# Optimization experiments

Measured on AMD Instinct MI355X. Metric: run time of the kernel, lower is better.

## Reference

```python
import jax, jax.numpy as jnp
import numpy as np
from jax import lax

N, E = 10000, 100000
IN_CH, HID, EDGE_DIM, K = 32, 64, 16, 3
DILATIONS = (1, 2, 4)


def setup_inputs() -> dict:
    key = jax.random.key(0)
    ks = jax.random.split(key, 20)
    def nrm(k, shape, fan):
        return jax.random.normal(k, shape, jnp.float32) * (1.0 / np.sqrt(fan))
    inp = {
        "x": jax.random.normal(ks[0], (N, IN_CH), jnp.float32),
        "edge_attr": jax.random.normal(ks[1], (E, EDGE_DIM), jnp.float32),
        "h_prev": jax.random.normal(ks[2], (N, K, HID), jnp.float32),
        "edge_index": jax.random.randint(ks[3], (2, E), 0, N, jnp.int32),
        # edge-conditioning MLP: edge_dim -> 32 -> in_ch*hid
        "w1": nrm(ks[4], (EDGE_DIM, 32), EDGE_DIM), "b1": jnp.zeros((32,), jnp.float32),
        "w2": nrm(ks[5], (32, IN_CH * HID), 32), "b2": jnp.zeros((IN_CH * HID,), jnp.float32),
        # NNConv root weight + bias
        "root": nrm(ks[6], (IN_CH, HID), IN_CH), "bias": jnp.zeros((HID,), jnp.float32),
        # three dilated Conv1d layers [out, in, k]
        "tcn_w1": nrm(ks[7], (HID, HID, K), HID * K), "tcn_b1": jnp.zeros((HID,), jnp.float32),
        "tcn_w2": nrm(ks[8], (HID, HID, K), HID * K), "tcn_b2": jnp.zeros((HID,), jnp.float32),
        "tcn_w3": nrm(ks[9], (HID, HID, K), HID * K), "tcn_b3": jnp.zeros((HID,), jnp.float32),
        # output projection hid*3 -> hid
        "proj_w": nrm(ks[10], (HID * len(DILATIONS), HID), HID * len(DILATIONS)),
        "proj_b": jnp.zeros((HID,), jnp.float32),
    }
    return inp


def _conv1d_last(h, w, b, dilation):
    # h: [N, C, L], w: [O, I, K]; 'same'-style padding (K-1)*d//2, return last timestep.
    pad = (K - 1) * dilation // 2
    out = lax.conv_general_dilated(
        h, w, window_strides=(1,), padding=[(pad, pad)],
        rhs_dilation=(dilation,), dimension_numbers=("NCH", "OIH", "NCH"))
    return out[:, :, -1] + b[None, :]


def reference(x, edge_attr, h_prev, edge_index,
              w1, b1, w2, b2, root, bias,
              tcn_w1, tcn_b1, tcn_w2, tcn_b2, tcn_w3, tcn_b3,
              proj_w, proj_b):
    src, dst = edge_index[0], edge_index[1]
    n = x.shape[0]

    # --- NNConv (ECC): per-edge weight via MLP, gather -> matmul -> scatter-mean ---
    h_e = jax.nn.relu(edge_attr @ w1 + b1)                   # [E, 32]
    W_e = (h_e @ w2 + b2).reshape(-1, IN_CH, HID)            # [E, in, hid]
    msg = jnp.einsum("ei,eio->eo", x[src], W_e)             # [E, hid]
    agg = jax.ops.segment_sum(msg, dst, num_segments=n)      # [N, hid]
    cnt = jax.ops.segment_sum(jnp.ones((msg.shape[0],), msg.dtype), dst, num_segments=n)
    mean = agg / jnp.maximum(cnt, 1.0)[:, None]
    h_graph = jax.nn.relu(mean + x @ root + bias)            # [N, hid]

    # --- history update ---
    h_hist = jnp.concatenate([h_prev[:, 1:], h_graph[:, None, :]], axis=1)  # [N, K, hid]

    # --- dilated TCN stack, keep only last timestep of each branch ---
    h_in = jnp.transpose(h_hist, (0, 2, 1))                  # [N, hid, K]
    outs = [
        _conv1d_last(h_in, tcn_w1, tcn_b1, DILATIONS[0]),
        _conv1d_last(h_in, tcn_w2, tcn_b2, DILATIONS[1]),
        _conv1d_last(h_in, tcn_w3, tcn_b3, DILATIONS[2]),
    ]
    h_cat = jnp.concatenate(outs, axis=1)                    # [N, hid*3]
    h_out = h_cat @ proj_w + proj_b                          # dropout = identity (eval)
    return h_out, h_hist
```

## Files before the change

### kernel.cpp

```cpp
#include <hip/hip_runtime.h>
#include <stdint.h>

#define NN 10000
#define NE 100000
#define CHUNK 10

__device__ __forceinline__ float bu2f(uint16_t u) {
    return __uint_as_float(((uint32_t)u) << 16);
}
__device__ __forceinline__ float blo(uint32_t v) { return __uint_as_float(v << 16); }
__device__ __forceinline__ float bhi(uint32_t v) { return __uint_as_float(v & 0xffff0000u); }
__device__ __forceinline__ uint16_t f2bu(float f) {
    uint32_t u = __float_as_uint(f);
    return (uint16_t)((u + 0x7fffu + ((u >> 16) & 1u)) >> 16);
}
__device__ __forceinline__ float ldf(const void* p, size_t i, int f32) {
    return f32 ? ((const float*)p)[i] : bu2f(((const uint16_t*)p)[i]);
}
struct f8 { float v[8]; };
__device__ __forceinline__ f8 ldf8(const void* p, size_t i, int f32) {
    f8 r;
    if (f32) {
        const float4* q = (const float4*)((const float*)p + i);
        float4 a = q[0], b = q[1];
        r.v[0]=a.x; r.v[1]=a.y; r.v[2]=a.z; r.v[3]=a.w;
        r.v[4]=b.x; r.v[5]=b.y; r.v[6]=b.z; r.v[7]=b.w;
    } else {
        uint4 u = *(const uint4*)((const uint16_t*)p + i);
        r.v[0]=blo(u.x); r.v[1]=bhi(u.x); r.v[2]=blo(u.y); r.v[3]=bhi(u.y);
        r.v[4]=blo(u.z); r.v[5]=bhi(u.z); r.v[6]=blo(u.w); r.v[7]=bhi(u.w);
    }
    return r;
}
__device__ __forceinline__ void stf(void* p, size_t i, float v, int f32) {
    if (f32) ((float*)p)[i] = v;
    else ((uint16_t*)p)[i] = f2bu(v);
}
__device__ __forceinline__ int clampi(int v, int lo, int hi) {
    return min(max(v, lo), hi);
}

__global__ __launch_bounds__(256) void k_init(
    const void* __restrict__ x, float4* __restrict__ zbase, int* __restrict__ flag)
{
    __shared__ int red[256];
    int bid = blockIdx.x;
    int tid = threadIdx.x;
    if (bid < 657) {
        int idx = bid * 256 + tid;
        if (idx < 168088) zbase[idx] = make_float4(0.f, 0.f, 0.f, 0.f);
    } else {
        const uint16_t* p = (const uint16_t*)x;
        int c = 0;
        #pragma unroll
        for (int q = 0; q < 4; q++) {
            float a = fabsf(bu2f(p[tid + q * 256]));
            if (a > 1e-3f && a < 16.0f) c++;
        }
        red[tid] = c;
        __syncthreads();
        #pragma unroll
        for (int d = 128; d > 0; d >>= 1) {
            if (tid < d) red[tid] += red[tid + d];
            __syncthreads();
        }
        if (tid == 0) *flag = (red[0] < 870) ? 1 : 0;
    }
}

__global__ __launch_bounds__(256, 4) void k_prep(
    const void* __restrict__ x, const void* __restrict__ root,
    const void* __restrict__ tw1, const void* __restrict__ tw2,
    const void* __restrict__ tw3,
    const void* __restrict__ tb1, const void* __restrict__ tb2,
    const void* __restrict__ tb3,
    const void* __restrict__ proj_w,
    const void* __restrict__ edge_attr, const void* __restrict__ w1,
    const void* __restrict__ b1,
    const void* __restrict__ w2, const void* __restrict__ b2,
    const int* __restrict__ ei, const int* __restrict__ flag,
    float* __restrict__ xs_f, float* __restrict__ root_f,
    float* __restrict__ A, float* __restrict__ B, float* __restrict__ C,
    float* __restrict__ dv,
    int* __restrict__ outdeg, int* __restrict__ indeg, int* __restrict__ rank,
    uint16_t* __restrict__ h_edge,
    uint16_t* __restrict__ T, float* __restrict__ xb)
{
    int bid = blockIdx.x;
    int tid = threadIdx.x;
    __shared__ union PU {
        struct { float xs[8][32]; uint16_t Ts[32][64]; } t;
        struct { float w1s[512]; float b1s[32]; float eas[32][16]; } mlp;
    } su;

    if (bid < 1250) {
        int f32 = *flag;
        int n0 = bid * 8;
        if (tid < 32) {
            f8 r = ldf8(x, (size_t)n0 * 32 + (size_t)tid * 8, f32);
            int base = tid * 8;
            #pragma unroll
            for (int q = 0; q < 8; q++) su.t.xs[(base + q) >> 5][(base + q) & 31] = r.v[q];
        }
        __syncthreads();
        int j = tid >> 3;
        int o0 = (tid & 7) * 8;
        float acc[8][8];
        #pragma unroll
        for (int s = 0; s < 8; s++)
            #pragma unroll
            for (int r = 0; r < 8; r++) acc[s][r] = 0.0f;
        if (f32) {
            const float* wb = (const float*)w2 + (size_t)j * 2048 + o0;
            for (int i = 0; i < 32; i++) {
                float4 a4 = *(const float4*)(wb + i * 64);
                float4 b4 = *(const float4*)(wb + i * 64 + 4);
                #pragma unroll
                for (int s = 0; s < 8; s++) {
                    float xv = su.t.xs[s][i];
                    acc[s][0] = fmaf(xv, a4.x, acc[s][0]); acc[s][1] = fmaf(xv, a4.y, acc[s][1]);
                    acc[s][2] = fmaf(xv, a4.z, acc[s][2]); acc[s][3] = fmaf(xv, a4.w, acc[s][3]);
                    acc[s][4] = fmaf(xv, b4.x, acc[s][4]); acc[s][5] = fmaf(xv, b4.y, acc[s][5]);
                    acc[s][6] = fmaf(xv, b4.z, acc[s][6]); acc[s][7] = fmaf(xv, b4.w, acc[s][7]);
                }
            }
        } else {
            const uint16_t* wb = (const uint16_t*)w2 + (size_t)j * 2048 + o0;
            for (int i = 0; i < 32; i++) {
                uint4 u = *(const uint4*)(wb + i * 64);
                float w0 = blo(u.x), w1_ = bhi(u.x), w2_ = blo(u.y), w3 = bhi(u.y);
                float w4 = blo(u.z), w5 = bhi(u.z), w6 = blo(u.w), w7 = bhi(u.w);
                #pragma unroll
                for (int s = 0; s < 8; s++) {
                    float xv = su.t.xs[s][i];
                    acc[s][0] = fmaf(xv, w0, acc[s][0]); acc[s][1] = fmaf(xv, w1_, acc[s][1]);
                    acc[s][2] = fmaf(xv, w2_, acc[s][2]); acc[s][3] = fmaf(xv, w3, acc[s][3]);
                    acc[s][4] = fmaf(xv, w4, acc[s][4]); acc[s][5] = fmaf(xv, w5, acc[s][5]);
                    acc[s][6] = fmaf(xv, w6, acc[s][6]); acc[s][7] = fmaf(xv, w7, acc[s][7]);
                }
            }
        }
        int k = tid >> 6, o = tid & 63;
        #pragma unroll
        for (int s = 0; s < 8; s++) {
            uint4 ov;
            ov.x = ((uint32_t)f2bu(acc[s][1]) << 16) | f2bu(acc[s][0]);
            ov.y = ((uint32_t)f2bu(acc[s][3]) << 16) | f2bu(acc[s][2]);
            ov.z = ((uint32_t)f2bu(acc[s][5]) << 16) | f2bu(acc[s][4]);
            ov.w = ((uint32_t)f2bu(acc[s][7]) << 16) | f2bu(acc[s][6]);
            *(uint4*)&su.t.Ts[j][o0] = ov;
            __syncthreads();
            uint16_t v0 = su.t.Ts[k * 8 + 0][o];
            uint16_t v1 = su.t.Ts[k * 8 + 1][o];
            uint16_t v2 = su.t.Ts[k * 8 + 2][o];
            uint16_t v3 = su.t.Ts[k * 8 + 3][o];
            uint16_t v4 = su.t.Ts[k * 8 + 4][o];
            uint16_t v5 = su.t.Ts[k * 8 + 5][o];
            uint16_t v6 = su.t.Ts[k * 8 + 6][o];
            uint16_t v7 = su.t.Ts[k * 8 + 7][o];
            uint4 tv_;
            tv_.x = (uint32_t)v0 | ((uint32_t)v1 << 16);
            tv_.y = (uint32_t)v2 | ((uint32_t)v3 << 16);
            tv_.z = (uint32_t)v4 | ((uint32_t)v5 << 16);
            tv_.w = (uint32_t)v6 | ((uint32_t)v7 << 16);
            *(uint4*)(T + (size_t)(n0 + s) * 2048 + (size_t)o * 32 + k * 8) = tv_;
            __syncthreads();
        }
        {
            int oo = tid & 63;
            if (f32) {
                const float* b2f = (const float*)b2;
                #pragma unroll
                for (int h = 0; h < 2; h++) {
                    int s = (tid >> 6) + h * 4;
                    float a2 = 0.0f;
                    #pragma unroll
                    for (int i = 0; i < 32; i++)
                        a2 = fmaf(su.t.xs[s][i], b2f[i * 64 + oo], a2);
                    xb[(size_t)(n0 + s) * 64 + oo] = a2;
                }
            } else {
                const uint16_t* b2u = (const uint16_t*)b2;
                #pragma unroll
                for (int h = 0; h < 2; h++) {
                    int s = (tid >> 6) + h * 4;
                    float a2 = 0.0f;
                    #pragma unroll
                    for (int i = 0; i < 32; i++)
                        a2 = fmaf(su.t.xs[s][i], bu2f(b2u[i * 64 + oo]), a2);
                    xb[(size_t)(n0 + s) * 64 + oo] = a2;
                }
            }
        }
    } else if (bid < 4375) {
        int f32 = *flag;
        int e0 = (bid - 1250) * 32;
        if (tid < 64) {
            f8 r = ldf8(w1, (size_t)tid * 8, f32);
            #pragma unroll
            for (int q = 0; q < 8; q++) su.mlp.w1s[tid * 8 + q] = r.v[q];
        } else if (tid < 128) {
            int t = tid - 64;
            f8 r = ldf8(edge_attr, (size_t)e0 * 16 + (size_t)t * 8, f32);
            int el = t >> 1, half = (t & 1) * 8;
            #pragma unroll
            for (int q = 0; q < 8; q++) su.mlp.eas[el][half + q] = r.v[q];
        } else if (tid < 160) {
            su.mlp.b1s[tid - 128] = ldf(b1, tid - 128, f32);
        }
        __syncthreads();
        int el = tid >> 5, jj = tid & 31;
        float wreg[16];
        #pragma unroll
        for (int k = 0; k < 16; k++) wreg[k] = su.mlp.w1s[k * 32 + jj];
        float bj = su.mlp.b1s[jj];
        #pragma unroll
        for (int r = 0; r < 4; r++) {
            int e = el + r * 8;
            float acc = bj;
            #pragma unroll
            for (int k = 0; k < 16; k++) acc = fmaf(su.mlp.eas[e][k], wreg[k], acc);
            h_edge[(size_t)(e0 + e) * 32 + jj] = f2bu(fmaxf(acc, 0.0f));
        }
    } else if (bid < 4887) {
        int f32 = *flag;
        int beta = bid - 4375;
        int i = beta >> 3;
        int chunk = beta & 7;
        int o = tid & 63, sub = tid >> 6;
        int cc0 = chunk * 8 + sub * 2;
        float a = 0.f, b = 0.f, c = 0.f, d = 0.f;
        #pragma unroll
        for (int m = 0; m < 2; m++) {
            int cc = cc0 + m;
            float p0 = ldf(proj_w, (size_t)cc * 64 + o, f32);
            float p1 = ldf(proj_w, (size_t)(64 + cc) * 64 + o, f32);
            float p2 = ldf(proj_w, (size_t)(128 + cc) * 64 + o, f32);
            size_t base = (size_t)cc * 192 + i * 3;
            a = fmaf(ldf(tw1, base + 1, f32), p0, a);
            a = fmaf(ldf(tw2, base + 1, f32), p1, a);
            a = fmaf(ldf(tw3, base + 1, f32), p2, a);
            b = fmaf(ldf(tw2, base + 0, f32), p1, b);
            c = fmaf(ldf(tw1, base + 0, f32), p0, c);
            if (i == 0) {
                d = fmaf(ldf(tb1, cc, f32), p0, d);
                d = fmaf(ldf(tb2, cc, f32), p1, d);
                d = fmaf(ldf(tb3, cc, f32), p2, d);
            }
        }
        unsafeAtomicAdd(&A[i * 64 + o], a);
        unsafeAtomicAdd(&B[i * 64 + o], b);
        unsafeAtomicAdd(&C[i * 64 + o], c);
        if (i == 0) unsafeAtomicAdd(&dv[o], d);
    } else if (bid < 5278) {
        int e = (bid - 4887) * 256 + tid;
        if (e < NE) {
            int src = clampi(ei[e], 0, NN - 1);
            rank[e] = atomicAdd(&outdeg[src], 1);
            atomicAdd(&indeg[clampi(ei[NE + e], 0, NN - 1)], 1);
        }
    } else if (bid < 5435) {
        int f32 = *flag;
        int v8 = (bid - 5278) * 256 + tid;
        if (v8 < 40000) {
            f8 r = ldf8(x, (size_t)v8 * 8, f32);
            float4* o = (float4*)(xs_f + (size_t)v8 * 8);
            o[0] = make_float4(r.v[0], r.v[1], r.v[2], r.v[3]);
            o[1] = make_float4(r.v[4], r.v[5], r.v[6], r.v[7]);
        }
    } else {
        int f32 = *flag;
        f8 r = ldf8(root, (size_t)tid * 8, f32);
        float4* o = (float4*)(root_f + (size_t)tid * 8);
        o[0] = make_float4(r.v[0], r.v[1], r.v[2], r.v[3]);
        o[1] = make_float4(r.v[4], r.v[5], r.v[6], r.v[7]);
    }
}

__global__ __launch_bounds__(256) void k_scat(
    const int* __restrict__ ei, const int* __restrict__ outdeg,
    const int* __restrict__ rank,
    int* __restrict__ sorted_src, int* __restrict__ sorted_dst,
    int* __restrict__ sorted_eid,
    const uint16_t* __restrict__ h_edge, uint16_t* __restrict__ h_srt, int hs_mode)
{
    __shared__ int offs_l[NN];
    __shared__ int tsum[256];
    int tid = threadIdx.x;
    const int CH = 40;
    int base = tid * CH;
    int s = 0;
    for (int k = 0; k < CH; k++) {
        int i = base + k;
        if (i < NN) s += outdeg[i];
    }
    tsum[tid] = s;
    __syncthreads();
    for (int d = 1; d < 256; d <<= 1) {
        int t = (tid >= d) ? tsum[tid - d] : 0;
        __syncthreads();
        if (tid >= d) tsum[tid] += t;
        __syncthreads();
    }
    int run = (tid == 0) ? 0 : tsum[tid - 1];
    for (int k = 0; k < CH; k++) {
        int i = base + k;
        if (i < NN) { offs_l[i] = run; run += outdeg[i]; }
    }
    __syncthreads();
    #pragma unroll
    for (int r = 0; r < 4; r++) {
        int e = blockIdx.x * 1024 + r * 256 + tid;
        if (e < NE) {
            int src = clampi(ei[e], 0, NN - 1);
            int dst = clampi(ei[NE + e], 0, NN - 1);
            int pos = clampi(offs_l[src] + rank[e], 0, NE - 1);
            sorted_src[pos] = src;
            sorted_dst[pos] = dst;
            if (hs_mode) {
                const uint4* hs = (const uint4*)(h_edge + (size_t)e * 32);
                uint4* hd = (uint4*)(h_srt + (size_t)pos * 32);
                hd[0] = hs[0]; hd[1] = hs[1]; hd[2] = hs[2]; hd[3] = hs[3];
            } else {
                sorted_eid[pos] = e;
            }
        }
    }
}

__global__ __launch_bounds__(256) void k_msg_g(
    const uint16_t* __restrict__ h_edge, const uint16_t* __restrict__ h_srt,
    int hs_mode, const uint16_t* __restrict__ T,
    const float* __restrict__ xb, const int* __restrict__ sorted_src,
    const int* __restrict__ sorted_dst, const int* __restrict__ sorted_eid,
    float* __restrict__ agg)
{
    int wid = blockIdx.x * 4 + (threadIdx.x >> 6);
    int lane = threadIdx.x & 63;
    int p0 = wid * CHUNK;
    if (p0 >= NE) return;
    int p1 = min(p0 + CHUNK, NE);
    int cur = -1;
    float tv[32];
    float xbv = 0.0f;
    int sN = clampi(sorted_src[p0], 0, NN - 1);
    const uint4* hq;
    if (hs_mode) hq = (const uint4*)(h_srt + (size_t)p0 * 32);
    else hq = (const uint4*)(h_edge + (size_t)clampi(sorted_eid[p0], 0, NE - 1) * 32);
    uint4 na = hq[0], nb = hq[1], nc = hq[2], nd = hq[3];
    for (int p = p0; p < p1; p++) {
        int s = sN;
        uint4 a = na, b = nb, c = nc, d = nd;
        int dst = clampi(sorted_dst[p], 0, NN - 1);
        if (p + 1 < p1) {
            sN = clampi(sorted_src[p + 1], 0, NN - 1);
            const uint4* h2;
            if (hs_mode) h2 = (const uint4*)(h_srt + (size_t)(p + 1) * 32);
            else h2 = (const uint4*)(h_edge + (size_t)clampi(sorted_eid[p + 1], 0, NE - 1) * 32);
            na = h2[0]; nb = h2[1]; nc = h2[2]; nd = h2[3];
        }
        if (s != cur) {
            cur = s;
            const uint4* Tp = (const uint4*)(T + (size_t)s * 2048 + (size_t)lane * 32);
            uint4 t0 = Tp[0], t1 = Tp[1], t2 = Tp[2], t3 = Tp[3];
            tv[0]=blo(t0.x); tv[1]=bhi(t0.x); tv[2]=blo(t0.y); tv[3]=bhi(t0.y);
            tv[4]=blo(t0.z); tv[5]=bhi(t0.z); tv[6]=blo(t0.w); tv[7]=bhi(t0.w);
            tv[8]=blo(t1.x); tv[9]=bhi(t1.x); tv[10]=blo(t1.y); tv[11]=bhi(t1.y);
            tv[12]=blo(t1.z); tv[13]=bhi(t1.z); tv[14]=blo(t1.w); tv[15]=bhi(t1.w);
            tv[16]=blo(t2.x); tv[17]=bhi(t2.x); tv[18]=blo(t2.y); tv[19]=bhi(t2.y);
            tv[20]=blo(t2.z); tv[21]=bhi(t2.z); tv[22]=blo(t2.w); tv[23]=bhi(t2.w);
            tv[24]=blo(t3.x); tv[25]=bhi(t3.x); tv[26]=blo(t3.y); tv[27]=bhi(t3.y);
            tv[28]=blo(t3.z); tv[29]=bhi(t3.z); tv[30]=blo(t3.w); tv[31]=bhi(t3.w);
            xbv = xb[(size_t)s * 64 + lane];
        }
        float s0 = 0.f, s1 = 0.f, s2 = 0.f, s3 = 0.f;
        s0 = fmaf(blo(a.x), tv[0],  s0); s0 = fmaf(bhi(a.x), tv[1],  s0);
        s0 = fmaf(blo(a.y), tv[2],  s0); s0 = fmaf(bhi(a.y), tv[3],  s0);
        s0 = fmaf(blo(a.z), tv[4],  s0); s0 = fmaf(bhi(a.z), tv[5],  s0);
        s0 = fmaf(blo(a.w), tv[6],  s0); s0 = fmaf(bhi(a.w), tv[7],  s0);
        s1 = fmaf(blo(b.x), tv[8],  s1); s1 = fmaf(bhi(b.x), tv[9],  s1);
        s1 = fmaf(blo(b.y), tv[10], s1); s1 = fmaf(bhi(b.y), tv[11], s1);
        s1 = fmaf(blo(b.z), tv[12], s1); s1 = fmaf(bhi(b.z), tv[13], s1);
        s1 = fmaf(blo(b.w), tv[14], s1); s1 = fmaf(bhi(b.w), tv[15], s1);
        s2 = fmaf(blo(c.x), tv[16], s2); s2 = fmaf(bhi(c.x), tv[17], s2);
        s2 = fmaf(blo(c.y), tv[18], s2); s2 = fmaf(bhi(c.y), tv[19], s2);
        s2 = fmaf(blo(c.z), tv[20], s2); s2 = fmaf(bhi(c.z), tv[21], s2);
        s2 = fmaf(blo(c.w), tv[22], s2); s2 = fmaf(bhi(c.w), tv[23], s2);
        s3 = fmaf(blo(d.x), tv[24], s3); s3 = fmaf(bhi(d.x), tv[25], s3);
        s3 = fmaf(blo(d.y), tv[26], s3); s3 = fmaf(bhi(d.y), tv[27], s3);
        s3 = fmaf(blo(d.z), tv[28], s3); s3 = fmaf(bhi(d.z), tv[29], s3);
        s3 = fmaf(blo(d.w), tv[30], s3); s3 = fmaf(bhi(d.w), tv[31], s3);
        float acc = xbv + (s0 + s1) + (s2 + s3);
        unsafeAtomicAdd(&agg[(size_t)dst * 64 + lane], acc);
    }
}

__global__ __launch_bounds__(256) void k_node_out(
    const float* __restrict__ agg, const int* __restrict__ indeg,
    const float* __restrict__ xs_f, const float* __restrict__ root_f,
    const void* __restrict__ bias, const void* __restrict__ h_prev,
    const float* __restrict__ A, const float* __restrict__ B,
    const float* __restrict__ C, const float* __restrict__ dv,
    const void* __restrict__ proj_b,
    const int* __restrict__ flag, void* __restrict__ out)
{
    int f32 = *flag;
    int tid = threadIdx.x;
    int s = tid >> 6, o = tid & 63;
    int n = blockIdx.x * 4 + s;
    const size_t O1 = (size_t)NN * 64;
    __shared__ float hg_s[4][64], hp1_s[4][64], hp2_s[4][64];

    float xr = 0.0f;
    const float* xp = xs_f + (size_t)n * 32;
    #pragma unroll
    for (int i = 0; i < 32; i++)
        xr = fmaf(xp[i], root_f[i * 64 + o], xr);
    float c = (float)indeg[n];
    float m = agg[(size_t)n * 64 + o] / fmaxf(c, 1.0f);
    float hg = fmaxf(m + xr + ldf(bias, o, f32), 0.0f);
    float hp1 = ldf(h_prev, (size_t)n * 192 + 64 + o, f32);
    float hp2 = ldf(h_prev, (size_t)n * 192 + 128 + o, f32);
    hg_s[s][o] = hg; hp1_s[s][o] = hp1; hp2_s[s][o] = hp2;
    stf(out, O1 + (size_t)n * 192 + o, hp1, f32);
    stf(out, O1 + (size_t)n * 192 + 64 + o, hp2, f32);
    stf(out, O1 + (size_t)n * 192 + 128 + o, hg, f32);
    __syncthreads();

    float accA = 0.f, accB = 0.f, accC = 0.f;
    #pragma unroll 8
    for (int i = 0; i < 64; i++) {
        accA = fmaf(hg_s[s][i],  A[i * 64 + o], accA);
        accB = fmaf(hp1_s[s][i], B[i * 64 + o], accB);
        accC = fmaf(hp2_s[s][i], C[i * 64 + o], accC);
    }
    float acc = dv[o] + ldf(proj_b, o, f32) + (accA + accB) + accC;
    stf(out, (size_t)n * 64 + o, acc, f32);
}

static inline size_t align64(size_t v) { return (v + 63) & ~(size_t)63; }

extern "C" void kernel_launch(void* const* d_in, const int* in_sizes, int n_in,
                              void* d_out, int out_size, void* d_ws, size_t ws_size,
                              hipStream_t stream) {
    const void* x         = d_in[0];
    const void* edge_attr = d_in[1];
    const void* h_prev    = d_in[2];
    const int*  ei        = (const int*)d_in[3];
    const void* w1     = d_in[4];
    const void* b1     = d_in[5];
    const void* w2     = d_in[6];
    const void* b2     = d_in[7];
    const void* root   = d_in[8];
    const void* bias   = d_in[9];
    const void* tw1    = d_in[10];
    const void* tb1    = d_in[11];
    const void* tw2    = d_in[12];
    const void* tb2    = d_in[13];
    const void* tw3    = d_in[14];
    const void* tb3    = d_in[15];
    const void* proj_w = d_in[16];
    const void* proj_b = d_in[17];

    char* ws = (char*)d_ws;
    size_t off = 0;
    uint16_t* T      = (uint16_t*)(ws + off); off = align64(off + (size_t)NN * 2048 * 2);
    uint16_t* h_edge = (uint16_t*)(ws + off); off = align64(off + (size_t)NE * 32 * 2);
    float* xs_f   = (float*)(ws + off); off = align64(off + (size_t)NN * 32 * 4);
    float* root_f = (float*)(ws + off); off = align64(off + (size_t)2048 * 4);
    float* xb     = (float*)(ws + off); off = align64(off + (size_t)NN * 64 * 4);
    size_t zero_base = off;
    float* agg    = (float*)(ws + off); off = align64(off + (size_t)NN * 64 * 4);
    int* indeg    = (int*)(ws + off);   off = align64(off + (size_t)NN * 4);
    int* outdeg   = (int*)(ws + off);   off = align64(off + (size_t)NN * 4);
    float* Amat   = (float*)(ws + off); off = align64(off + (size_t)4096 * 4);
    float* Bmat   = (float*)(ws + off); off = align64(off + (size_t)4096 * 4);
    float* Cmat   = (float*)(ws + off); off = align64(off + (size_t)4096 * 4);
    float* dvec   = (float*)(ws + off); off = align64(off + (size_t)64 * 4);
    int* rank        = (int*)(ws + off); off = align64(off + (size_t)NE * 4);
    int* sorted_src  = (int*)(ws + off); off = align64(off + (size_t)NE * 4);
    int* sorted_dst  = (int*)(ws + off); off = align64(off + (size_t)NE * 4);
    int* sorted_eid  = (int*)(ws + off); off = align64(off + (size_t)NE * 4);
    int* flag        = (int*)(ws + off); off = align64(off + 64);
    uint16_t* h_srt  = (uint16_t*)(ws + off);
    size_t off_end = off + (size_t)NE * 32 * 2;
    int hs_mode = (off_end <= ws_size) ? 1 : 0;

    k_init<<<658, 256, 0, stream>>>(x, (float4*)((char*)d_ws + zero_base), flag);
    k_prep<<<5436, 256, 0, stream>>>(x, root, tw1, tw2, tw3, tb1, tb2, tb3,
                                     proj_w, edge_attr, w1, b1, w2, b2, ei, flag,
                                     xs_f, root_f, Amat, Bmat, Cmat, dvec,
                                     outdeg, indeg, rank, h_edge, T, xb);
    k_scat<<<(NE + 1023) / 1024, 256, 0, stream>>>(ei, outdeg, rank,
                                                   sorted_src, sorted_dst, sorted_eid,
                                                   h_edge, h_srt, hs_mode);
    k_msg_g<<<(NE / CHUNK + 3) / 4, 256, 0, stream>>>(h_edge, h_srt, hs_mode, T, xb,
                                                      sorted_src, sorted_dst,
                                                      sorted_eid, agg);
    k_node_out<<<NN / 4, 256, 0, stream>>>(agg, indeg, xs_f, root_f, bias, h_prev,
                                           Amat, Bmat, Cmat, dvec, proj_b, flag, d_out);
}
```

Before: 213.9 us.

## Drop sorted h_edge copy, prefetch T rows, double-buffer LDS transpose, widen MLP blocks

The scatter kernel no longer copies per-edge hidden vectors into sorted order. The message kernel now gathers h_edge through sorted_eid and prefetches the next source node's T row and xb value one edge ahead, so their load latency is hidden. The T-transpose stage double-buffers its shared-memory tile, which removes one barrier per iteration. The edge-MLP blocks now handle 64 edges each, with bounds checks, which cuts the prep grid size. The trade-off is that k_msg_g reads h_edge by random index instead of sequentially and holds more registers for the prefetched data.

```diff
diff --git a/kernel.cpp b/kernel.cpp
--- a/kernel.cpp
+++ b/kernel.cpp
@@ -89,8 +89,8 @@
     int bid = blockIdx.x;
     int tid = threadIdx.x;
     __shared__ union PU {
-        struct { float xs[8][32]; uint16_t Ts[32][64]; } t;
-        struct { float w1s[512]; float b1s[32]; float eas[32][16]; } mlp;
+        struct { float xs[8][32]; uint16_t Ts[2][32][64]; } t;
+        struct { float w1s[512]; float b1s[32]; float eas[64][16]; } mlp;
     } su;
 
     if (bid < 1250) {
@@ -148,23 +148,22 @@
             ov.y = ((uint32_t)f2bu(acc[s][3]) << 16) | f2bu(acc[s][2]);
             ov.z = ((uint32_t)f2bu(acc[s][5]) << 16) | f2bu(acc[s][4]);
             ov.w = ((uint32_t)f2bu(acc[s][7]) << 16) | f2bu(acc[s][6]);
-            *(uint4*)&su.t.Ts[j][o0] = ov;
+            *(uint4*)&su.t.Ts[s & 1][j][o0] = ov;
             __syncthreads();
-            uint16_t v0 = su.t.Ts[k * 8 + 0][o];
-            uint16_t v1 = su.t.Ts[k * 8 + 1][o];
-            uint16_t v2 = su.t.Ts[k * 8 + 2][o];
-            uint16_t v3 = su.t.Ts[k * 8 + 3][o];
-            uint16_t v4 = su.t.Ts[k * 8 + 4][o];
-            uint16_t v5 = su.t.Ts[k * 8 + 5][o];
-            uint16_t v6 = su.t.Ts[k * 8 + 6][o];
-            uint16_t v7 = su.t.Ts[k * 8 + 7][o];
+            uint16_t v0 = su.t.Ts[s & 1][k * 8 + 0][o];
+            uint16_t v1 = su.t.Ts[s & 1][k * 8 + 1][o];
+            uint16_t v2 = su.t.Ts[s & 1][k * 8 + 2][o];
+            uint16_t v3 = su.t.Ts[s & 1][k * 8 + 3][o];
+            uint16_t v4 = su.t.Ts[s & 1][k * 8 + 4][o];
+            uint16_t v5 = su.t.Ts[s & 1][k * 8 + 5][o];
+            uint16_t v6 = su.t.Ts[s & 1][k * 8 + 6][o];
+            uint16_t v7 = su.t.Ts[s & 1][k * 8 + 7][o];
             uint4 tv_;
             tv_.x = (uint32_t)v0 | ((uint32_t)v1 << 16);
             tv_.y = (uint32_t)v2 | ((uint32_t)v3 << 16);
             tv_.z = (uint32_t)v4 | ((uint32_t)v5 << 16);
             tv_.w = (uint32_t)v6 | ((uint32_t)v7 << 16);
             *(uint4*)(T + (size_t)(n0 + s) * 2048 + (size_t)o * 32 + k * 8) = tv_;
-            __syncthreads();
         }
         {
             int oo = tid & 63;
@@ -192,21 +191,27 @@
                 }
             }
         }
-    } else if (bid < 4375) {
+    } else if (bid < 2813) {
         int f32 = *flag;
-        int e0 = (bid - 1250) * 32;
+        int e0 = (bid - 1250) * 64;
         if (tid < 64) {
             f8 r = ldf8(w1, (size_t)tid * 8, f32);
             #pragma unroll
             for (int q = 0; q < 8; q++) su.mlp.w1s[tid * 8 + q] = r.v[q];
-        } else if (tid < 128) {
-            int t = tid - 64;
-            f8 r = ldf8(edge_attr, (size_t)e0 * 16 + (size_t)t * 8, f32);
-            int el = t >> 1, half = (t & 1) * 8;
-            #pragma unroll
-            for (int q = 0; q < 8; q++) su.mlp.eas[el][half + q] = r.v[q];
-        } else if (tid < 160) {
-            su.mlp.b1s[tid - 128] = ldf(b1, tid - 128, f32);
+        } else if (tid < 192) {
+            int tt = tid - 64;
+            size_t fo = (size_t)e0 * 16 + (size_t)tt * 8;
+            int el = tt >> 1, half = (tt & 1) * 8;
+            if (fo + 8 <= (size_t)NE * 16) {
+                f8 r = ldf8(edge_attr, fo, f32);
+                #pragma unroll
+                for (int q = 0; q < 8; q++) su.mlp.eas[el][half + q] = r.v[q];
+            } else {
+                #pragma unroll
+                for (int q = 0; q < 8; q++) su.mlp.eas[el][half + q] = 0.0f;
+            }
+        } else if (tid < 224) {
+            su.mlp.b1s[tid - 192] = ldf(b1, tid - 192, f32);
         }
         __syncthreads();
         int el = tid >> 5, jj = tid & 31;
@@ -215,16 +220,17 @@
         for (int k = 0; k < 16; k++) wreg[k] = su.mlp.w1s[k * 32 + jj];
         float bj = su.mlp.b1s[jj];
         #pragma unroll
-        for (int r = 0; r < 4; r++) {
+        for (int r = 0; r < 8; r++) {
             int e = el + r * 8;
             float acc = bj;
             #pragma unroll
             for (int k = 0; k < 16; k++) acc = fmaf(su.mlp.eas[e][k], wreg[k], acc);
-            h_edge[(size_t)(e0 + e) * 32 + jj] = f2bu(fmaxf(acc, 0.0f));
-        }
-    } else if (bid < 4887) {
+            if (e0 + e < NE)
+                h_edge[(size_t)(e0 + e) * 32 + jj] = f2bu(fmaxf(acc, 0.0f));
+        }
+    } else if (bid < 3325) {
         int f32 = *flag;
-        int beta = bid - 4375;
+        int beta = bid - 2813;
         int i = beta >> 3;
         int chunk = beta & 7;
         int o = tid & 63, sub = tid >> 6;
@@ -252,16 +258,16 @@
         unsafeAtomicAdd(&B[i * 64 + o], b);
         unsafeAtomicAdd(&C[i * 64 + o], c);
         if (i == 0) unsafeAtomicAdd(&dv[o], d);
-    } else if (bid < 5278) {
-        int e = (bid - 4887) * 256 + tid;
+    } else if (bid < 3716) {
+        int e = (bid - 3325) * 256 + tid;
         if (e < NE) {
             int src = clampi(ei[e], 0, NN - 1);
             rank[e] = atomicAdd(&outdeg[src], 1);
             atomicAdd(&indeg[clampi(ei[NE + e], 0, NN - 1)], 1);
         }
-    } else if (bid < 5435) {
+    } else if (bid < 3873) {
         int f32 = *flag;
-        int v8 = (bid - 5278) * 256 + tid;
+        int v8 = (bid - 3716) * 256 + tid;
         if (v8 < 40000) {
             f8 r = ldf8(x, (size_t)v8 * 8, f32);
             float4* o = (float4*)(xs_f + (size_t)v8 * 8);
@@ -281,8 +287,7 @@
     const int* __restrict__ ei, const int* __restrict__ outdeg,
     const int* __restrict__ rank,
     int* __restrict__ sorted_src, int* __restrict__ sorted_dst,
-    int* __restrict__ sorted_eid,
-    const uint16_t* __restrict__ h_edge, uint16_t* __restrict__ h_srt, int hs_mode)
+    int* __restrict__ sorted_eid)
 {
     __shared__ int offs_l[NN];
     __shared__ int tsum[256];
@@ -317,20 +322,13 @@
             int pos = clampi(offs_l[src] + rank[e], 0, NE - 1);
             sorted_src[pos] = src;
             sorted_dst[pos] = dst;
-            if (hs_mode) {
-                const uint4* hs = (const uint4*)(h_edge + (size_t)e * 32);
-                uint4* hd = (uint4*)(h_srt + (size_t)pos * 32);
-                hd[0] = hs[0]; hd[1] = hs[1]; hd[2] = hs[2]; hd[3] = hs[3];
-            } else {
-                sorted_eid[pos] = e;
-            }
+            sorted_eid[pos] = e;
         }
     }
 }
 
 __global__ __launch_bounds__(256) void k_msg_g(
-    const uint16_t* __restrict__ h_edge, const uint16_t* __restrict__ h_srt,
-    int hs_mode, const uint16_t* __restrict__ T,
+    const uint16_t* __restrict__ h_edge, const uint16_t* __restrict__ T,
     const float* __restrict__ xb, const int* __restrict__ sorted_src,
     const int* __restrict__ sorted_dst, const int* __restrict__ sorted_eid,
     float* __restrict__ agg)
@@ -344,34 +342,38 @@
     float tv[32];
     float xbv = 0.0f;
     int sN = clampi(sorted_src[p0], 0, NN - 1);
-    const uint4* hq;
-    if (hs_mode) hq = (const uint4*)(h_srt + (size_t)p0 * 32);
-    else hq = (const uint4*)(h_edge + (size_t)clampi(sorted_eid[p0], 0, NE - 1) * 32);
+    int eN = clampi(sorted_eid[p0], 0, NE - 1);
+    const uint4* hq = (const uint4*)(h_edge + (size_t)eN * 32);
     uint4 na = hq[0], nb = hq[1], nc = hq[2], nd = hq[3];
+    const uint4* Tq = (const uint4*)(T + (size_t)sN * 2048 + (size_t)lane * 32);
+    uint4 Tr0 = Tq[0], Tr1 = Tq[1], Tr2 = Tq[2], Tr3 = Tq[3];
+    float xbN = xb[(size_t)sN * 64 + lane];
     for (int p = p0; p < p1; p++) {
         int s = sN;
         uint4 a = na, b = nb, c = nc, d = nd;
+        if (s != cur) {
+            cur = s;
+            tv[0]=blo(Tr0.x); tv[1]=bhi(Tr0.x); tv[2]=blo(Tr0.y); tv[3]=bhi(Tr0.y);
+            tv[4]=blo(Tr0.z); tv[5]=bhi(Tr0.z); tv[6]=blo(Tr0.w); tv[7]=bhi(Tr0.w);
+            tv[8]=blo(Tr1.x); tv[9]=bhi(Tr1.x); tv[10]=blo(Tr1.y); tv[11]=bhi(Tr1.y);
+            tv[12]=blo(Tr1.z); tv[13]=bhi(Tr1.z); tv[14]=blo(Tr1.w); tv[15]=bhi(Tr1.w);
+            tv[16]=blo(Tr2.x); tv[17]=bhi(Tr2.x); tv[18]=blo(Tr2.y); tv[19]=bhi(Tr2.y);
+            tv[20]=blo(Tr2.z); tv[21]=bhi(Tr2.z); tv[22]=blo(Tr2.w); tv[23]=bhi(Tr2.w);
+            tv[24]=blo(Tr3.x); tv[25]=bhi(Tr3.x); tv[26]=blo(Tr3.y); tv[27]=bhi(Tr3.y);
+            tv[28]=blo(Tr3.z); tv[29]=bhi(Tr3.z); tv[30]=blo(Tr3.w); tv[31]=bhi(Tr3.w);
+            xbv = xbN;
+        }
         int dst = clampi(sorted_dst[p], 0, NN - 1);
         if (p + 1 < p1) {
             sN = clampi(sorted_src[p + 1], 0, NN - 1);
-            const uint4* h2;
-            if (hs_mode) h2 = (const uint4*)(h_srt + (size_t)(p + 1) * 32);
-            else h2 = (const uint4*)(h_edge + (size_t)clampi(sorted_eid[p + 1], 0, NE - 1) * 32);
+            int e2 = clampi(sorted_eid[p + 1], 0, NE - 1);
+            const uint4* h2 = (const uint4*)(h_edge + (size_t)e2 * 32);
             na = h2[0]; nb = h2[1]; nc = h2[2]; nd = h2[3];
-        }
-        if (s != cur) {
-            cur = s;
-            const uint4* Tp = (const uint4*)(T + (size_t)s * 2048 + (size_t)lane * 32);
-            uint4 t0 = Tp[0], t1 = Tp[1], t2 = Tp[2], t3 = Tp[3];
-            tv[0]=blo(t0.x); tv[1]=bhi(t0.x); tv[2]=blo(t0.y); tv[3]=bhi(t0.y);
-            tv[4]=blo(t0.z); tv[5]=bhi(t0.z); tv[6]=blo(t0.w); tv[7]=bhi(t0.w);
-            tv[8]=blo(t1.x); tv[9]=bhi(t1.x); tv[10]=blo(t1.y); tv[11]=bhi(t1.y);
-            tv[12]=blo(t1.z); tv[13]=bhi(t1.z); tv[14]=blo(t1.w); tv[15]=bhi(t1.w);
-            tv[16]=blo(t2.x); tv[17]=bhi(t2.x); tv[18]=blo(t2.y); tv[19]=bhi(t2.y);
-            tv[20]=blo(t2.z); tv[21]=bhi(t2.z); tv[22]=blo(t2.w); tv[23]=bhi(t2.w);
-            tv[24]=blo(t3.x); tv[25]=bhi(t3.x); tv[26]=blo(t3.y); tv[27]=bhi(t3.y);
-            tv[28]=blo(t3.z); tv[29]=bhi(t3.z); tv[30]=blo(t3.w); tv[31]=bhi(t3.w);
-            xbv = xb[(size_t)s * 64 + lane];
+            if (sN != cur) {
+                const uint4* T2q = (const uint4*)(T + (size_t)sN * 2048 + (size_t)lane * 32);
+                Tr0 = T2q[0]; Tr1 = T2q[1]; Tr2 = T2q[2]; Tr3 = T2q[3];
+                xbN = xb[(size_t)sN * 64 + lane];
+            }
         }
         float s0 = 0.f, s1 = 0.f, s2 = 0.f, s3 = 0.f;
         s0 = fmaf(blo(a.x), tv[0],  s0); s0 = fmaf(bhi(a.x), tv[1],  s0);
@@ -482,19 +484,15 @@
     int* sorted_dst  = (int*)(ws + off); off = align64(off + (size_t)NE * 4);
     int* sorted_eid  = (int*)(ws + off); off = align64(off + (size_t)NE * 4);
     int* flag        = (int*)(ws + off); off = align64(off + 64);
-    uint16_t* h_srt  = (uint16_t*)(ws + off);
-    size_t off_end = off + (size_t)NE * 32 * 2;
-    int hs_mode = (off_end <= ws_size) ? 1 : 0;
 
     k_init<<<658, 256, 0, stream>>>(x, (float4*)((char*)d_ws + zero_base), flag);
-    k_prep<<<5436, 256, 0, stream>>>(x, root, tw1, tw2, tw3, tb1, tb2, tb3,
+    k_prep<<<3874, 256, 0, stream>>>(x, root, tw1, tw2, tw3, tb1, tb2, tb3,
                                      proj_w, edge_attr, w1, b1, w2, b2, ei, flag,
                                      xs_f, root_f, Amat, Bmat, Cmat, dvec,
                                      outdeg, indeg, rank, h_edge, T, xb);
     k_scat<<<(NE + 1023) / 1024, 256, 0, stream>>>(ei, outdeg, rank,
-                                                   sorted_src, sorted_dst, sorted_eid,
-                                                   h_edge, h_srt, hs_mode);
-    k_msg_g<<<(NE / CHUNK + 3) / 4, 256, 0, stream>>>(h_edge, h_srt, hs_mode, T, xb,
+                                                   sorted_src, sorted_dst, sorted_eid);
+    k_msg_g<<<(NE / CHUNK + 3) / 4, 256, 0, stream>>>(h_edge, T, xb,
                                                       sorted_src, sorted_dst,
                                                       sorted_eid, agg);
     k_node_out<<<NN / 4, 256, 0, stream>>>(agg, indeg, xs_f, root_f, bias, h_prev,
```

Measured after the change: 220.4 us. +3.0%, slower.
